# Optimization experiments

Measured on AMD Instinct MI355X. Metric: run time of the kernel, lower is better.

The kernel has to match this reference:

```python
import jax, jax.numpy as jnp
import numpy as np

VOCAB, EMB, H, NL = 50257, 1024, 2048, 2


def _lstm_cell(x, h, c, Wih, Whh, bih, bhh):
    # x: [1, in], h/c: [1, H]; PyTorch gate order i, f, g, o
    gates = x @ Wih.T + bih + h @ Whh.T + bhh  # [1, 4H]
    i, f, g, o = jnp.split(gates, 4, axis=-1)
    c2 = jax.nn.sigmoid(f) * c + jax.nn.sigmoid(i) * jnp.tanh(g)
    h2 = jax.nn.sigmoid(o) * jnp.tanh(c2)
    return h2, c2


def setup_inputs() -> dict:
    key = jax.random.key(0)
    ks = jax.random.split(key, 12)
    s = 0.02  # keep gate pre-activations in a sane range
    return {
        "input_ids": jax.random.randint(ks[0], (1,), 0, VOCAB, dtype=jnp.int64),
        "h0": jax.random.normal(ks[1], (2 * NL, 1, H), jnp.float32) * 0.1,
        "c0": jax.random.normal(ks[2], (2 * NL, 1, H), jnp.float32) * 0.1,
        "emb": jax.random.normal(ks[3], (VOCAB, EMB), jnp.float32),
        "W_ih_l0": jax.random.normal(ks[4], (2, 4 * H, EMB), jnp.float32) * s,
        "W_hh_l0": jax.random.normal(ks[5], (2, 4 * H, H), jnp.float32) * s,
        "b_ih_l0": jax.random.normal(ks[6], (2, 4 * H), jnp.float32) * s,
        "b_hh_l0": jax.random.normal(ks[7], (2, 4 * H), jnp.float32) * s,
        "W_ih_l1": jax.random.normal(ks[8], (2, 4 * H, 2 * H), jnp.float32) * s,
        "W_hh_l1": jax.random.normal(ks[9], (2, 4 * H, H), jnp.float32) * s,
        "b_ih_l1": jax.random.normal(ks[10], (2, 4 * H), jnp.float32) * s,
        "b_hh_l1": jax.random.normal(ks[11], (2, 4 * H), jnp.float32) * s,
    }


def reference(input_ids, h0, c0, emb, W_ih_l0, W_hh_l0, b_ih_l0, b_hh_l0,
              W_ih_l1, W_hh_l1, b_ih_l1, b_hh_l1):
    # embedded = embedding(input).view(1, 1, -1) -> seq_len=1, batch=1
    x = emb[input_ids]  # [1, EMB]
    layers = [(W_ih_l0, W_hh_l0, b_ih_l0, b_hh_l0),
              (W_ih_l1, W_hh_l1, b_ih_l1, b_hh_l1)]
    h_out, c_out = [], []
    for l, (Wih, Whh, bih, bhh) in enumerate(layers):
        # seq_len == 1: fwd and bwd directions both see the single timestep
        hf, cf = _lstm_cell(x, h0[2 * l], c0[2 * l], Wih[0], Whh[0], bih[0], bhh[0])
        hb, cb = _lstm_cell(x, h0[2 * l + 1], c0[2 * l + 1], Wih[1], Whh[1], bih[1], bhh[1])
        h_out += [hf, hb]
        c_out += [cf, cb]
        x = jnp.concatenate([hf, hb], axis=-1)  # [1, 2H] input to next layer
    output = x[None]  # [1, 1, 2H] (seq, batch, 2*hidden)
    h_n = jnp.stack(h_out, axis=0)  # [2*NL, 1, H]
    c_n = jnp.stack(c_out, axis=0)
    return output, h_n, c_n
```

## Files before the change

kernel.cpp:

```cpp
#include <hip/hip_runtime.h>


#define HID 2048
#define G4H 8192

__device__ __forceinline__ float wave_reduce_sum(float v) {
    #pragma unroll
    for (int off = 32; off > 0; off >>= 1)
        v += __shfl_down(v, off, 64);
    return v;
}

template<int XDIM>
__global__ __launch_bounds__(256) void gates_kernel(
    const float* __restrict__ x,
    const int*   __restrict__ tok,
    const float* __restrict__ Wih,
    const float* __restrict__ Whh,
    const float* __restrict__ bih,
    const float* __restrict__ bhh,
    const float* __restrict__ h0,
    int h0_off,
    float* __restrict__ gates)
{
    const int wave = (int)((blockIdx.x * blockDim.x + threadIdx.x) >> 6);
    const int lane = (int)(threadIdx.x & 63);
    const int dir  = wave >> 13;
    const int r    = wave & (G4H - 1);

    if (tok) x += (size_t)tok[0] * XDIM;

    const float4* wih = (const float4*)(Wih + ((size_t)dir * G4H + r) * XDIM);
    const float4* whh = (const float4*)(Whh + ((size_t)dir * G4H + r) * HID);
    const float4* xv  = (const float4*)x;
    const float4* hv  = (const float4*)(h0 + (size_t)(h0_off + dir) * HID);

    float acc = 0.f;
    #pragma unroll
    for (int i = 0; i < XDIM / 4 / 64; ++i) {
        float4 w = wih[lane + i * 64];
        float4 b = xv [lane + i * 64];
        acc += w.x * b.x + w.y * b.y + w.z * b.z + w.w * b.w;
    }
    #pragma unroll
    for (int i = 0; i < HID / 4 / 64; ++i) {
        float4 w = whh[lane + i * 64];
        float4 b = hv [lane + i * 64];
        acc += w.x * b.x + w.y * b.y + w.z * b.z + w.w * b.w;
    }
    acc = wave_reduce_sum(acc);
    if (lane == 0) {
        int row = dir * G4H + r;
        gates[row] = acc + bih[row] + bhh[row];
    }
}

__device__ __forceinline__ float sigmoidf_(float v) {
    return 1.f / (1.f + expf(-v));
}

__global__ __launch_bounds__(256) void cell_kernel(
    const float* __restrict__ gates,
    const float* __restrict__ c0,
    int lo,
    float* __restrict__ hn,
    float* __restrict__ cn,
    float* __restrict__ xout)
{
    const int idx = (int)(blockIdx.x * blockDim.x + threadIdx.x);
    const int d = idx >> 11;
    const int j = idx & (HID - 1);

    const float* g = gates + d * G4H;
    float gi = g[j];
    float gf = g[HID + j];
    float gg = g[2 * HID + j];
    float go = g[3 * HID + j];

    float c_prev = c0[(size_t)(lo + d) * HID + j];
    float c2 = sigmoidf_(gf) * c_prev + sigmoidf_(gi) * tanhf(gg);
    float h2 = sigmoidf_(go) * tanhf(c2);

    hn[(size_t)(lo + d) * HID + j] = h2;
    cn[(size_t)(lo + d) * HID + j] = c2;
    xout[(size_t)d * HID + j] = h2;
}

extern "C" void kernel_launch(void* const* d_in, const int* in_sizes, int n_in,
                              void* d_out, int out_size, void* d_ws, size_t ws_size,
                              hipStream_t stream) {
    const int*   ids  = (const int*)  d_in[0];
    const float* h0   = (const float*)d_in[1];
    const float* c0   = (const float*)d_in[2];
    const float* emb  = (const float*)d_in[3];
    const float* Wih0 = (const float*)d_in[4];
    const float* Whh0 = (const float*)d_in[5];
    const float* bih0 = (const float*)d_in[6];
    const float* bhh0 = (const float*)d_in[7];
    const float* Wih1 = (const float*)d_in[8];
    const float* Whh1 = (const float*)d_in[9];
    const float* bih1 = (const float*)d_in[10];
    const float* bhh1 = (const float*)d_in[11];

    float* out   = (float*)d_out;
    float* gates = (float*)d_ws;
    float* x1    = gates + 2 * G4H;

    gates_kernel<1024><<<4096, 256, 0, stream>>>(emb, ids, Wih0, Whh0, bih0, bhh0, h0, 0, gates);
    cell_kernel<<<16, 256, 0, stream>>>(gates, c0, 0, out + 4096, out + 12288, x1);
    gates_kernel<4096><<<4096, 256, 0, stream>>>(x1, nullptr, Wih1, Whh1, bih1, bhh1, h0, 2, gates);
    cell_kernel<<<16, 256, 0, stream>>>(gates, c0, 2, out + 4096, out + 12288, out);
}
```

Before: 107.9 us.

## Hoist layer-1 recurrent matvec into first kernel alongside layer-0 gates

Computes the layer-1 hidden-to-hidden matvec (Whh1·h0 plus both biases) in the first kernel, which has no dependency on layer 0, writing a partial-gate buffer. The second-layer kernel then only processes the input-to-hidden weights and adds the partial sums. This moves independent weight streaming off the serial critical path between cell kernels and gives the first launch more parallel work. Total memory traffic stays the same and an extra workspace buffer is used.

```diff
diff --git a/kernel.cpp b/kernel.cpp
--- a/kernel.cpp
+++ b/kernel.cpp
@@ -11,16 +11,73 @@
     return v;
 }
 
-template<int XDIM>
-__global__ __launch_bounds__(256) void gates_kernel(
-    const float* __restrict__ x,
+__global__ __launch_bounds__(256) void phase1_kernel(
     const int*   __restrict__ tok,
-    const float* __restrict__ Wih,
-    const float* __restrict__ Whh,
-    const float* __restrict__ bih,
-    const float* __restrict__ bhh,
+    const float* __restrict__ emb,
+    const float* __restrict__ Wih0,
+    const float* __restrict__ Whh0,
+    const float* __restrict__ bih0,
+    const float* __restrict__ bhh0,
+    const float* __restrict__ Whh1,
+    const float* __restrict__ bih1,
+    const float* __restrict__ bhh1,
     const float* __restrict__ h0,
-    int h0_off,
+    float* __restrict__ gates0,
+    float* __restrict__ part1)
+{
+    const int wave = (int)((blockIdx.x * blockDim.x + threadIdx.x) >> 6);
+    const int lane = (int)(threadIdx.x & 63);
+
+    if (wave < 2 * G4H) {
+        const int dir = wave >> 13;
+        const int r   = wave & (G4H - 1);
+        const float*  x   = emb + (size_t)tok[0] * 1024;
+        const float4* wih = (const float4*)(Wih0 + ((size_t)dir * G4H + r) * 1024);
+        const float4* whh = (const float4*)(Whh0 + ((size_t)dir * G4H + r) * HID);
+        const float4* xv  = (const float4*)x;
+        const float4* hv  = (const float4*)(h0 + (size_t)dir * HID);
+
+        float acc = 0.f;
+        #pragma unroll
+        for (int i = 0; i < 1024 / 4 / 64; ++i) {
+            float4 w = wih[lane + i * 64], b = xv[lane + i * 64];
+            acc += w.x * b.x + w.y * b.y + w.z * b.z + w.w * b.w;
+        }
+        #pragma unroll
+        for (int i = 0; i < HID / 4 / 64; ++i) {
+            float4 w = whh[lane + i * 64], b = hv[lane + i * 64];
+            acc += w.x * b.x + w.y * b.y + w.z * b.z + w.w * b.w;
+        }
+        acc = wave_reduce_sum(acc);
+        if (lane == 0) {
+            int row = dir * G4H + r;
+            gates0[row] = acc + bih0[row] + bhh0[row];
+        }
+    } else {
+        const int w2  = wave - 2 * G4H;
+        const int dir = w2 >> 13;
+        const int r   = w2 & (G4H - 1);
+        const float4* whh = (const float4*)(Whh1 + ((size_t)dir * G4H + r) * HID);
+        const float4* hv  = (const float4*)(h0 + (size_t)(2 + dir) * HID);
+
+        float acc = 0.f;
+        #pragma unroll
+        for (int i = 0; i < HID / 4 / 64; ++i) {
+            float4 w = whh[lane + i * 64], b = hv[lane + i * 64];
+            acc += w.x * b.x + w.y * b.y + w.z * b.z + w.w * b.w;
+        }
+        acc = wave_reduce_sum(acc);
+        if (lane == 0) {
+            int row = dir * G4H + r;
+            part1[row] = acc + bih1[row] + bhh1[row];
+        }
+    }
+}
+
+__global__ __launch_bounds__(256) void phase2_kernel(
+    const float* __restrict__ x1,
+    const float* __restrict__ Wih1,
+    const float* __restrict__ part1,
     float* __restrict__ gates)
 {
     const int wave = (int)((blockIdx.x * blockDim.x + threadIdx.x) >> 6);
@@ -28,30 +85,19 @@
     const int dir  = wave >> 13;
     const int r    = wave & (G4H - 1);
 
-    if (tok) x += (size_t)tok[0] * XDIM;
-
-    const float4* wih = (const float4*)(Wih + ((size_t)dir * G4H + r) * XDIM);
-    const float4* whh = (const float4*)(Whh + ((size_t)dir * G4H + r) * HID);
-    const float4* xv  = (const float4*)x;
-    const float4* hv  = (const float4*)(h0 + (size_t)(h0_off + dir) * HID);
+    const float4* wih = (const float4*)(Wih1 + ((size_t)dir * G4H + r) * 4096);
+    const float4* xv  = (const float4*)x1;
 
     float acc = 0.f;
     #pragma unroll
-    for (int i = 0; i < XDIM / 4 / 64; ++i) {
-        float4 w = wih[lane + i * 64];
-        float4 b = xv [lane + i * 64];
-        acc += w.x * b.x + w.y * b.y + w.z * b.z + w.w * b.w;
-    }
-    #pragma unroll
-    for (int i = 0; i < HID / 4 / 64; ++i) {
-        float4 w = whh[lane + i * 64];
-        float4 b = hv [lane + i * 64];
+    for (int i = 0; i < 4096 / 4 / 64; ++i) {
+        float4 w = wih[lane + i * 64], b = xv[lane + i * 64];
         acc += w.x * b.x + w.y * b.y + w.z * b.z + w.w * b.w;
     }
     acc = wave_reduce_sum(acc);
     if (lane == 0) {
         int row = dir * G4H + r;
-        gates[row] = acc + bih[row] + bhh[row];
+        gates[row] = acc + part1[row];
     }
 }
 
@@ -102,12 +148,14 @@
     const float* bih1 = (const float*)d_in[10];
     const float* bhh1 = (const float*)d_in[11];
 
-    float* out   = (float*)d_out;
-    float* gates = (float*)d_ws;
-    float* x1    = gates + 2 * G4H;
+    float* out    = (float*)d_out;
+    float* gates  = (float*)d_ws;
+    float* part1  = gates + 2 * G4H;
+    float* x1     = part1 + 2 * G4H;
 
-    gates_kernel<1024><<<4096, 256, 0, stream>>>(emb, ids, Wih0, Whh0, bih0, bhh0, h0, 0, gates);
+    phase1_kernel<<<8192, 256, 0, stream>>>(ids, emb, Wih0, Whh0, bih0, bhh0,
+                                            Whh1, bih1, bhh1, h0, gates, part1);
     cell_kernel<<<16, 256, 0, stream>>>(gates, c0, 0, out + 4096, out + 12288, x1);
-    gates_kernel<4096><<<4096, 256, 0, stream>>>(x1, nullptr, Wih1, Whh1, bih1, bhh1, h0, 2, gates);
+    phase2_kernel<<<4096, 256, 0, stream>>>(x1, Wih1, part1, gates);
     cell_kernel<<<16, 256, 0, stream>>>(gates, c0, 2, out + 4096, out + 12288, out);
 }
```

Result: no change. 106.3 us (-1.5%).
